# Kernel optimization log

Hardware: AMD Instinct MI355X
Metric: run time of the kernel (lower is better)

## Reference

```python
import jax, jax.numpy as jnp
import numpy as np

B, T, D, H = 4, 2048, 1024, 16
Dh = D // H

def setup_inputs() -> dict:
    key = jax.random.key(0)
    ks = jax.random.split(key, 6)
    scale = 1.0 / np.sqrt(D)
    return {
        "x": jax.random.normal(ks[0], (B, T, D), dtype=jnp.float32),
        "W_q": jax.random.normal(ks[1], (D, D), dtype=jnp.float32) * scale,
        "W_k": jax.random.normal(ks[2], (D, D), dtype=jnp.float32) * scale,
        "W_v": jax.random.normal(ks[3], (D, D), dtype=jnp.float32) * scale,
        "W_o": jax.random.normal(ks[4], (D, D), dtype=jnp.float32) * scale,
        "b_o": jax.random.normal(ks[5], (D,), dtype=jnp.float32) * 0.02,
    }

def reference(x, W_q, W_k, W_v, W_o, b_o):
    # Linear weights stored torch-style (out, in): y = x @ W.T
    def split_heads(z):
        return z.reshape(B, T, H, Dh).transpose(0, 2, 1, 3)  # [B,H,T,Dh]
    q = split_heads(x @ W_q.T)
    k = split_heads(x @ W_k.T)
    v = split_heads(x @ W_v.T)
    scale = Dh ** -0.5
    attn = jnp.einsum('bhqd,bhkd->bhqk', q, k) * scale  # [B,H,T,T]
    causal = jnp.tril(jnp.ones((T, T), dtype=bool))
    attn = jnp.where(causal[None, None], attn, -jnp.inf)
    attn = jax.nn.softmax(attn, axis=-1)
    y = jnp.einsum('bhqk,bhkd->bhqd', attn, v)  # [B,H,T,Dh]
    y = y.transpose(0, 2, 1, 3).reshape(B, T, D)
    return y @ W_o.T + b_o
```

## Files before the change

kernel.cpp:

```cpp
#include <hip/hip_runtime.h>
#include <hip/hip_bf16.h>
#include <stdint.h>

#define B_   4
#define T_   2048
#define H_   16
#define MTOT (B_ * T_)
#define NQKV 3072
#define QSC  0.18033688f

typedef __attribute__((ext_vector_type(8))) __bf16 bf16x8;
typedef __attribute__((ext_vector_type(4))) float f32x4;
typedef __attribute__((ext_vector_type(16))) float f32x16;
typedef __attribute__((ext_vector_type(4))) float f4v;
typedef __attribute__((ext_vector_type(4))) unsigned short us4;
typedef __attribute__((ext_vector_type(8))) unsigned short us8;
typedef __attribute__((ext_vector_type(4))) unsigned int u32x4;

static __device__ __forceinline__ unsigned short f2bf(float f) {
  __hip_bfloat16 h = __float2bfloat16(f);
  return __builtin_bit_cast(unsigned short, h);
}

static __device__ __forceinline__ float fast_exp2(float x) {
#if __has_builtin(__builtin_amdgcn_exp2f)
  return __builtin_amdgcn_exp2f(x);
#else
  float r; asm("v_exp_f32 %0, %1" : "=v"(r) : "v"(x)); return r;
#endif
}

static __device__ __forceinline__ void async16(const void* g, void* l) {
  __builtin_amdgcn_global_load_lds(
      (const __attribute__((address_space(1))) void*)g,
      (__attribute__((address_space(3))) void*)l, 16, 0, 0);
}

#define XHALF(res, x, OP)                                  \
  {                                                        \
    float t1_ = (x), t2_ = (x);                            \
    asm("" : "+v"(t2_));                                   \
    asm("v_permlane32_swap_b32 %0, %1" : "+v"(t1_), "+v"(t2_)); \
    res = OP(t1_, t2_);                                    \
  }
static __device__ __forceinline__ float fadd_(float a, float b) { return a + b; }

__global__ __launch_bounds__(256) void cvt_all(
    const float* __restrict__ x, const float* __restrict__ Wq,
    const float* __restrict__ Wk, const float* __restrict__ Wv,
    const float* __restrict__ Wo, unsigned short* __restrict__ xb,
    unsigned short* __restrict__ wqkv, unsigned short* __restrict__ wo) {
  int i = blockIdx.x * blockDim.x + threadIdx.x;
  const float* s; unsigned short* d; int j;
  if (i < 2097152)      { s = x;  d = xb;             j = i; }
  else if (i < 2359296) { s = Wq; d = wqkv;           j = i - 2097152; }
  else if (i < 2621440) { s = Wk; d = wqkv + 1048576; j = i - 2359296; }
  else if (i < 2883584) { s = Wv; d = wqkv + 2097152; j = i - 2621440; }
  else                  { s = Wo; d = wo;             j = i - 2883584; }
  f4v v = reinterpret_cast<const f4v*>(s)[j];
  us4 o;
  o.x = f2bf(v.x); o.y = f2bf(v.y); o.z = f2bf(v.z); o.w = f2bf(v.w);
  reinterpret_cast<us4*>(d)[j] = o;
}

template <int MODE, int NT>
__global__ __launch_bounds__(256) void gemm_bt(
    const unsigned short* __restrict__ A,
    const unsigned short* __restrict__ Bw,
    unsigned short* __restrict__ Cb,
    float* __restrict__ Cf,
    const float* __restrict__ bias,
    int K, int N) {
  __shared__ __align__(16) unsigned short As[128 * 64];
  __shared__ __align__(16) unsigned short Bs[128 * 64];

  const int bid = blockIdx.x;
  const int xcd = bid & 7;
  const int loc = bid >> 3;
  const int m0 = (xcd * 8 + loc / NT) * 128;
  const int n0 = (loc % NT) * 128;

  const int t = threadIdx.x;
  const int lane = t & 63;
  const int w = t >> 6;
  const int lr = lane & 15;
  const int lg = lane >> 4;
  const int wm = w >> 1;
  const int wn = w & 1;

  f32x4 acc[4][4];
#pragma unroll
  for (int i = 0; i < 4; ++i)
#pragma unroll
    for (int j = 0; j < 4; ++j) acc[i][j] = (f32x4){0.f, 0.f, 0.f, 0.f};

  const int srow = t >> 3;
  const int gs = (t & 7) ^ ((t >> 3) & 7);
  const unsigned short* ga = A + (size_t)(m0 + srow) * K + gs * 8;
  const unsigned short* gb = Bw + (size_t)(n0 + srow) * K + gs * 8;

  const int rsw = lr & 7;

  for (int k0 = 0; k0 < K; k0 += 64) {
#pragma unroll
    for (int k = 0; k < 4; ++k) {
      async16(ga + (size_t)(k * 32) * K + k0, &As[(k * 256 + t) * 8]);
      async16(gb + (size_t)(k * 32) * K + k0, &Bs[(k * 256 + t) * 8]);
    }
    __syncthreads();

#pragma unroll
    for (int kk = 0; kk < 2; ++kk) {
      const int slot = ((kk * 4 + lg) ^ rsw) * 8;
      bf16x8 af[4], bfr[4];
#pragma unroll
      for (int mi = 0; mi < 4; ++mi)
        af[mi] = *(const bf16x8*)&As[(wm * 64 + mi * 16 + lr) * 64 + slot];
#pragma unroll
      for (int ni = 0; ni < 4; ++ni)
        bfr[ni] = *(const bf16x8*)&Bs[(wn * 64 + ni * 16 + lr) * 64 + slot];
#pragma unroll
      for (int mi = 0; mi < 4; ++mi)
#pragma unroll
        for (int ni = 0; ni < 4; ++ni)
          acc[mi][ni] = __builtin_amdgcn_mfma_f32_16x16x32_bf16(
              af[mi], bfr[ni], acc[mi][ni], 0, 0, 0);
    }
    __syncthreads();
  }

#pragma unroll
  for (int mi = 0; mi < 4; ++mi) {
    const int row = m0 + wm * 64 + mi * 16 + lg * 4;
#pragma unroll
    for (int ni = 0; ni < 4; ++ni) {
      const int col = n0 + wn * 64 + ni * 16 + lr;
#pragma unroll
      for (int r = 0; r < 4; ++r) {
        if (MODE == 1) {
          Cf[(size_t)(row + r) * N + col] = acc[mi][ni][r] + bias[col];
        } else {
          float v = acc[mi][ni][r];
          if (col < 1024) v *= QSC;
          Cb[(size_t)(row + r) * N + col] = f2bf(v);
        }
      }
    }
  }
}

__global__ __launch_bounds__(256, 4) void attn_kernel(
    const unsigned short* __restrict__ qkv, unsigned short* __restrict__ ob) {
  const int bid = blockIdx.x;
  const int pair = bid & 63;
  const int g = bid >> 6;
  const int rnd = g >> 2, idx = g & 3;
  const int qg = (rnd == 0) ? (15 - idx)
               : (rnd == 1) ? (8 + idx)
               : (rnd == 2) ? (7 - idx) : idx;
  const int b = pair >> 4;
  const int h = pair & 15;
  const int t = threadIdx.x;
  const int w = t >> 6;
  const int lane = t & 63;
  const int l31 = lane & 31;
  const int hi = lane >> 5;

  const int q0w = qg * 128 + w * 32;
  const int myBound = 2 * qg + (w >> 1);
  const int NT = 2 * qg + 2;

  __shared__ __align__(16) unsigned short Ks[2][64 * 64];
  __shared__ __align__(16) unsigned short Vs[2][64 * 64];

  const size_t rowbase = (size_t)(b * T_) * NQKV;

  bf16x8 Qf[4];
  {
    const unsigned short* qp =
        qkv + rowbase + (size_t)(q0w + l31) * NQKV + h * 64 + hi * 8;
#pragma unroll
    for (int m = 0; m < 4; ++m) Qf[m] = *(const bf16x8*)(qp + m * 16);
  }

  const int kr = t >> 3;
  const int ks = t & 7;
  const unsigned short* kbase =
      qkv + rowbase + 1024 + h * 64 + (ks ^ (kr & 7)) * 8 + (size_t)kr * NQKV;
  const int kvr = t >> 2;
  const int dc2 = (t & 3) * 2;
  const unsigned short* vbase =
      qkv + rowbase + 2048 + h * 64 + dc2 * 8 + (size_t)kvr * NQKV;

  float m_i = -INFINITY, l_i = 0.f;
  f32x16 o[2];
#pragma unroll
  for (int r = 0; r < 16; ++r) { o[0][r] = 0.f; o[1][r] = 0.f; }

#define VSCATTER(Vb, v0, v1)                                       \
  {                                                                \
    _Pragma("unroll") for (int i = 0; i < 8; ++i) {                \
      const int s0 = ((kvr >> 3) ^ dc2 ^ i) & 7;                   \
      const int s1 = ((kvr >> 3) ^ (dc2 + 1) ^ i) & 7;             \
      (Vb)[(dc2 * 8 + i) * 64 + s0 * 8 + (kvr & 7)] = (v0)[i];     \
      (Vb)[((dc2 + 1) * 8 + i) * 64 + s1 * 8 + (kvr & 7)] = (v1)[i]; \
    }                                                              \
  }

  {
    async16(kbase, &Ks[0][t * 8]);
    async16(kbase + (size_t)32 * NQKV, &Ks[0][2048 + t * 8]);
    us8 v0 = *(const us8*)vbase;
    us8 v1 = *(const us8*)(vbase + 8);
    VSCATTER(&Vs[0][0], v0, v1);
  }

  int cur = 0;
  for (int kt = 0; kt < NT; ++kt) {
    __syncthreads();

    const bool pf = (kt + 1 < NT);
    us8 v0, v1;
    if (pf) {
      const size_t off = (size_t)(kt + 1) * 64 * NQKV;
      async16(kbase + off, &Ks[cur ^ 1][t * 8]);
      async16(kbase + off + (size_t)32 * NQKV, &Ks[cur ^ 1][2048 + t * 8]);
      v0 = *(const us8*)(vbase + off);
      v1 = *(const us8*)(vbase + off + 8);
    }

    if (kt <= myBound) {
      const unsigned short* Kb = Ks[cur];
      const unsigned short* Vb = Vs[cur];

      f32x16 a0, a1;
#pragma unroll
      for (int r = 0; r < 16; ++r) { a0[r] = 0.f; a1[r] = 0.f; }
      {
        const int rb0 = l31 * 64;
        const int rb1 = (32 + l31) * 64;
        const int r7 = l31 & 7;
        __builtin_amdgcn_s_setprio(1);
#pragma unroll
        for (int m = 0; m < 4; ++m) {
          const int c = (((m << 1) | hi) ^ r7) * 8;
          bf16x8 kf0 = *(const bf16x8*)&Kb[rb0 + c];
          bf16x8 kf1 = *(const bf16x8*)&Kb[rb1 + c];
          a0 = __builtin_amdgcn_mfma_f32_32x32x16_bf16(kf0, Qf[m], a0, 0, 0, 0);
          a1 = __builtin_amdgcn_mfma_f32_32x32x16_bf16(kf1, Qf[m], a1, 0, 0, 0);
        }
        __builtin_amdgcn_s_setprio(0);
      }

      if (kt == myBound) {
        const int qglob = q0w + l31;
#pragma unroll
        for (int r = 0; r < 16; ++r) {
          const int kvb = kt * 64 + (r & 3) + ((r >> 2) << 3) + (hi << 2);
          if (kvb > qglob) a0[r] = -INFINITY;
          if (kvb + 32 > qglob) a1[r] = -INFINITY;
        }
      }

      float m8[8];
#pragma unroll
      for (int j = 0; j < 8; ++j)
        m8[j] = fmaxf(fmaxf(a0[j], a0[j + 8]), fmaxf(a1[j], a1[j + 8]));
      float pp = fmaxf(fmaxf(fmaxf(m8[0], m8[4]), fmaxf(m8[1], m8[5])),
                       fmaxf(fmaxf(m8[2], m8[6]), fmaxf(m8[3], m8[7])));
      float pmax;
      XHALF(pmax, pp, fmaxf);
      if (__any(pmax > m_i + 8.f)) {
        const float mnew = fmaxf(m_i, pmax);
        const float al = fast_exp2(m_i - mnew);
        m_i = mnew;
        l_i *= al;
#pragma unroll
        for (int r = 0; r < 16; ++r) { o[0][r] *= al; o[1][r] *= al; }
      }

#pragma unroll
      for (int r = 0; r < 16; ++r) {
        a0[r] = fast_exp2(a0[r] - m_i);
        a1[r] = fast_exp2(a1[r] - m_i);
      }
      float s8[8];
#pragma unroll
      for (int j = 0; j < 8; ++j)
        s8[j] = (a0[j] + a0[j + 8]) + (a1[j] + a1[j + 8]);
      float rp = ((s8[0] + s8[1]) + (s8[2] + s8[3])) +
                 ((s8[4] + s8[5]) + (s8[6] + s8[7]));
      float rs;
      XHALF(rs, rp, fadd_);
      l_i += rs;

      bf16x8 Pf[4];
#pragma unroll
      for (int m = 0; m < 4; ++m) {
        const int rb2 = (m & 1) * 8;
        uint32_t u0, u1, u2, u3;
        const f32x16& s = (m >> 1) ? a1 : a0;
        asm("v_cvt_pk_bf16_f32 %0, %1, %2" : "=v"(u0) : "v"(s[rb2 + 0]), "v"(s[rb2 + 1]));
        asm("v_cvt_pk_bf16_f32 %0, %1, %2" : "=v"(u1) : "v"(s[rb2 + 2]), "v"(s[rb2 + 3]));
        asm("v_cvt_pk_bf16_f32 %0, %1, %2" : "=v"(u2) : "v"(s[rb2 + 4]), "v"(s[rb2 + 5]));
        asm("v_cvt_pk_bf16_f32 %0, %1, %2" : "=v"(u3) : "v"(s[rb2 + 6]), "v"(s[rb2 + 7]));
        asm("v_permlane32_swap_b32 %0, %1" : "+v"(u0), "+v"(u2));
        asm("v_permlane32_swap_b32 %0, %1" : "+v"(u1), "+v"(u3));
        u32x4 pw = {u0, u1, u2, u3};
        Pf[m] = __builtin_bit_cast(bf16x8, pw);
      }

      __builtin_amdgcn_s_setprio(1);
#pragma unroll
      for (int dt = 0; dt < 2; ++dt) {
        const int d = dt * 32 + l31;
        const int base = d * 64;
        const int dsw = ((d >> 3) ^ d) & 7;
#pragma unroll
        for (int m = 0; m < 4; ++m) {
          bf16x8 vf = *(const bf16x8*)&Vb[base + ((((m << 1) | hi) ^ dsw) & 7) * 8];
          o[dt] = __builtin_amdgcn_mfma_f32_32x32x16_bf16(vf, Pf[m], o[dt], 0, 0, 0);
        }
      }
      __builtin_amdgcn_s_setprio(0);
    }

    if (pf) VSCATTER(&Vs[cur ^ 1][0], v0, v1);
    cur ^= 1;
  }

  const float rl = 1.0f / l_i;
#pragma unroll
  for (int dt = 0; dt < 2; ++dt) {
    float s[16];
#pragma unroll
    for (int r = 0; r < 16; ++r) s[r] = o[dt][r] * rl;
    uint32_t u[8];
#pragma unroll
    for (int p = 0; p < 8; ++p)
      asm("v_cvt_pk_bf16_f32 %0, %1, %2" : "=v"(u[p]) : "v"(s[2 * p]), "v"(s[2 * p + 1]));
    asm("v_permlane32_swap_b32 %0, %1" : "+v"(u[0]), "+v"(u[2]));
    asm("v_permlane32_swap_b32 %0, %1" : "+v"(u[1]), "+v"(u[3]));
    asm("v_permlane32_swap_b32 %0, %1" : "+v"(u[4]), "+v"(u[6]));
    asm("v_permlane32_swap_b32 %0, %1" : "+v"(u[5]), "+v"(u[7]));
    unsigned short* op =
        ob + (size_t)(b * T_ + q0w + l31) * 1024 + h * 64 + dt * 32 + hi * 8;
    u32x4 c0 = {u[0], u[1], u[2], u[3]};
    u32x4 c1 = {u[4], u[5], u[6], u[7]};
    *(u32x4*)op = c0;
    *(u32x4*)(op + 16) = c1;
  }
}

extern "C" void kernel_launch(void* const* d_in, const int* in_sizes, int n_in,
                              void* d_out, int out_size, void* d_ws,
                              size_t ws_size, hipStream_t stream) {
  const float* x = (const float*)d_in[0];
  const float* Wq = (const float*)d_in[1];
  const float* Wk = (const float*)d_in[2];
  const float* Wv = (const float*)d_in[3];
  const float* Wo = (const float*)d_in[4];
  const float* bo = (const float*)d_in[5];
  float* out = (float*)d_out;

  char* ws = (char*)d_ws;
  unsigned short* xb   = (unsigned short*)(ws + 0);
  unsigned short* wqkv = (unsigned short*)(ws + 16777216);
  unsigned short* wo   = (unsigned short*)(ws + 23068672);
  unsigned short* qkv  = (unsigned short*)(ws + 25165824);
  unsigned short* ob   = (unsigned short*)(ws + 75497472);
  if (ws_size < 92274688u) return;

  cvt_all<<<12288, 256, 0, stream>>>(x, Wq, Wk, Wv, Wo, xb, wqkv, wo);

  gemm_bt<0, 24><<<1536, 256, 0, stream>>>(
      xb, wqkv, qkv, nullptr, nullptr, 1024, NQKV);

  attn_kernel<<<dim3(1024), 256, 0, stream>>>(qkv, ob);

  gemm_bt<1, 8><<<512, 256, 0, stream>>>(
      ob, wo, nullptr, out, bo, 1024, 1024);
}
```

Measured before the change: 170.5 us.

## Triple-buffer K tiles in attention and prefetch them two iterations ahead

The attention kernel's K shared-memory buffer grows from two to three slots, so K tiles are fetched asynchronously two iterations ahead, while V still goes through registers one iteration ahead. The top-of-loop __syncthreads becomes an end-of-iteration lgkmcnt wait plus a raw s_barrier fenced by sched_barrier. The goal is to hide global-load latency for K and cut barrier overhead. In exchange, shared memory per block grows and launch bounds drop from 4 to 3 blocks per CU. Correctness relies on in-order vmcnt completion: the V load wait is what guarantees the async K loads have landed.

```diff
diff --git a/kernel.cpp b/kernel.cpp
--- a/kernel.cpp
+++ b/kernel.cpp
@@ -35,6 +35,8 @@
       (const __attribute__((address_space(1))) void*)g,
       (__attribute__((address_space(3))) void*)l, 16, 0, 0);
 }
+
+#define SB0() __builtin_amdgcn_sched_barrier(0)
 
 #define XHALF(res, x, OP)                                  \
   {                                                        \
@@ -149,7 +151,7 @@
   }
 }
 
-__global__ __launch_bounds__(256, 4) void attn_kernel(
+__global__ __launch_bounds__(256, 3) void attn_kernel(
     const unsigned short* __restrict__ qkv, unsigned short* __restrict__ ob) {
   const int bid = blockIdx.x;
   const int pair = bid & 63;
@@ -170,8 +172,8 @@
   const int myBound = 2 * qg + (w >> 1);
   const int NT = 2 * qg + 2;
 
-  __shared__ __align__(16) unsigned short Ks[2][64 * 64];
-  __shared__ __align__(16) unsigned short Vs[2][64 * 64];
+  __shared__ __align__(16) unsigned short KsAll[3 * 64 * 64];
+  __shared__ __align__(16) unsigned short VsAll[3 * 64 * 64];
 
   const size_t rowbase = (size_t)(b * T_) * NQKV;
 
@@ -208,30 +210,40 @@
   }
 
   {
-    async16(kbase, &Ks[0][t * 8]);
-    async16(kbase + (size_t)32 * NQKV, &Ks[0][2048 + t * 8]);
+    async16(kbase, &KsAll[t * 8]);
+    async16(kbase + (size_t)32 * NQKV, &KsAll[2048 + t * 8]);
     us8 v0 = *(const us8*)vbase;
     us8 v1 = *(const us8*)(vbase + 8);
-    VSCATTER(&Vs[0][0], v0, v1);
-  }
-
-  int cur = 0;
+    async16(kbase + (size_t)64 * NQKV, &KsAll[4096 + t * 8]);
+    async16(kbase + (size_t)96 * NQKV, &KsAll[4096 + 2048 + t * 8]);
+    VSCATTER(&VsAll[0], v0, v1);
+    asm volatile("s_waitcnt lgkmcnt(0)" ::: "memory");
+    SB0();
+    __builtin_amdgcn_s_barrier();
+    SB0();
+  }
+
+  int bcur = 0, bnx1 = 4096, bnx2 = 8192;
+
   for (int kt = 0; kt < NT; ++kt) {
-    __syncthreads();
-
-    const bool pf = (kt + 1 < NT);
-    us8 v0, v1;
-    if (pf) {
-      const size_t off = (size_t)(kt + 1) * 64 * NQKV;
-      async16(kbase + off, &Ks[cur ^ 1][t * 8]);
-      async16(kbase + off + (size_t)32 * NQKV, &Ks[cur ^ 1][2048 + t * 8]);
-      v0 = *(const us8*)(vbase + off);
-      v1 = *(const us8*)(vbase + off + 8);
+    const bool haveV = (kt + 1 < NT);
+    const bool haveK = (kt + 2 < NT);
+
+    us8 w0, w1;
+    if (haveV) {
+      const size_t off1 = (size_t)(kt + 1) * 64 * NQKV;
+      w0 = *(const us8*)(vbase + off1);
+      w1 = *(const us8*)(vbase + off1 + 8);
+    }
+    if (haveK) {
+      const size_t off2 = (size_t)(kt + 2) * 64 * NQKV;
+      async16(kbase + off2, &KsAll[bnx2 + t * 8]);
+      async16(kbase + off2 + (size_t)32 * NQKV, &KsAll[bnx2 + 2048 + t * 8]);
     }
 
     if (kt <= myBound) {
-      const unsigned short* Kb = Ks[cur];
-      const unsigned short* Vb = Vs[cur];
+      const unsigned short* Kb = &KsAll[bcur];
+      const unsigned short* Vb = &VsAll[bcur];
 
       f32x16 a0, a1;
 #pragma unroll
@@ -325,8 +337,14 @@
       __builtin_amdgcn_s_setprio(0);
     }
 
-    if (pf) VSCATTER(&Vs[cur ^ 1][0], v0, v1);
-    cur ^= 1;
+    if (haveV) VSCATTER(&VsAll[bnx1], w0, w1);
+
+    asm volatile("s_waitcnt lgkmcnt(0)" ::: "memory");
+    SB0();
+    __builtin_amdgcn_s_barrier();
+    SB0();
+
+    const int tmp = bcur; bcur = bnx1; bnx1 = bnx2; bnx2 = tmp;
   }
 
   const float rl = 1.0f / l_i;
```

After: 172.5 us. About the same (+1.2%).
